# Kernel optimization log

Hardware: AMD Instinct MI355X
Metric: run time of the kernel (lower is better)

Reference implementation:

```python
import jax, jax.numpy as jnp
import numpy as np

LN_EPS = 1e-5


def setup_inputs() -> dict:
    key = jax.random.key(0)
    ks = jax.random.split(key, 6)
    B, S, D = 4, 4096, 2048
    Db = D // 4  # bottleneck_dim = n_embd // compression_ratio
    hidden = jax.random.normal(ks[0], (B, S, D), dtype=jnp.float32)
    # LayerNorm params (torch defaults: gamma=1, beta=0)
    ln_gamma = jnp.ones((D,), dtype=jnp.float32)
    ln_beta = jnp.zeros((D,), dtype=jnp.float32)
    # Linear weights, torch default init: U(-1/sqrt(fan_in), 1/sqrt(fan_in))
    bd_lim = 1.0 / np.sqrt(D)
    W_down = jax.random.uniform(ks[1], (D, Db), minval=-bd_lim, maxval=bd_lim, dtype=jnp.float32)
    b_down = jax.random.uniform(ks[2], (Db,), minval=-bd_lim, maxval=bd_lim, dtype=jnp.float32)
    bu_lim = 1.0 / np.sqrt(Db)
    W_up = jax.random.uniform(ks[3], (Db, D), minval=-bu_lim, maxval=bu_lim, dtype=jnp.float32)
    b_up = jax.random.uniform(ks[4], (D,), minval=-bu_lim, maxval=bu_lim, dtype=jnp.float32)
    alpha = jnp.array(0.01, dtype=jnp.float32)
    return {
        "hidden": hidden,
        "ln_gamma": ln_gamma,
        "ln_beta": ln_beta,
        "W_down": W_down,
        "b_down": b_down,
        "W_up": W_up,
        "b_up": b_up,
        "alpha": alpha,
        "layer_idx": 0,
    }


def reference(hidden, ln_gamma, ln_beta, W_down, b_down, W_up, b_up, alpha, layer_idx):
    # LayerNorm over last dim
    mu = jnp.mean(hidden, axis=-1, keepdims=True)
    var = jnp.mean(jnp.square(hidden - mu), axis=-1, keepdims=True)
    h_norm = (hidden - mu) * jax.lax.rsqrt(var + LN_EPS) * ln_gamma + ln_beta
    # down-proj -> SiLU -> up-proj   [b s d] @ [d k] -> [b s k] -> [b s d]
    z = jnp.einsum("bsd,dk->bsk", h_norm, W_down) + b_down
    z = jax.nn.silu(z)
    bottleneck_out = jnp.einsum("bsk,kd->bsd", z, W_up) + b_up
    # alpha-gated residual
    return hidden + alpha * (bottleneck_out - hidden)
```

## Files before the change

kernel.cpp:

```cpp
#include <hip/hip_runtime.h>

typedef __bf16 bf16x8 __attribute__((ext_vector_type(8)));
typedef __bf16 bf16x4 __attribute__((ext_vector_type(4)));
typedef float f32x4 __attribute__((ext_vector_type(4)));

#define S_BARRIER() asm volatile("s_barrier" ::: "memory")
#define WAITCNT_VM(n) asm volatile("s_waitcnt vmcnt(" #n ")" ::: "memory")
#define WAITCNT_LGKM0() asm volatile("s_waitcnt lgkmcnt(0)" ::: "memory")

__global__ __launch_bounds__(256) void prep_ln_kernel(
    const float* __restrict__ Wd, __bf16* __restrict__ Wtd,
    const float* __restrict__ Wu, __bf16* __restrict__ Wtu,
    const float* __restrict__ x, const float* __restrict__ g,
    const float* __restrict__ be, __bf16* __restrict__ y,
    int D, int Db, int ntiles) {
    if ((int)blockIdx.x < ntiles) {
        const float* W;
        __bf16* Wt;
        int K, N, tile;
        const int ntile_d = (Db / 32) * (D / 32);
        if ((int)blockIdx.x < ntile_d) {
            W = Wd; Wt = Wtd; K = D; N = Db; tile = blockIdx.x;
        } else {
            W = Wu; Wt = Wtu; K = Db; N = D; tile = blockIdx.x - ntile_d;
        }
        const int tn = tile % (N / 32), tk = tile / (N / 32);
        const int n0 = tn * 32, k0 = tk * 32;
        __shared__ float t[32][33];
        const int c = threadIdx.x & 31, r0 = threadIdx.x >> 5;
#pragma unroll
        for (int r = r0; r < 32; r += 8)
            t[r][c] = W[(size_t)(k0 + r) * N + n0 + c];
        __syncthreads();
#pragma unroll
        for (int r = r0; r < 32; r += 8)
            Wt[(size_t)(n0 + r) * K + k0 + c] = (__bf16)t[c][r];
        return;
    }
    const int t = threadIdx.x;
    const int wv = t >> 6, ln = t & 63;
    const size_t row = (size_t)(blockIdx.x - ntiles) * 4 + wv;
    const float4* xr = (const float4*)(x + row * (size_t)D);
    const int nv = D >> 3;
    float s = 0.f, ss = 0.f;
    for (int i = ln; i < nv; i += 64) {
        float4 v0 = xr[i * 2], v1 = xr[i * 2 + 1];
        s += v0.x + v0.y + v0.z + v0.w + v1.x + v1.y + v1.z + v1.w;
        ss += v0.x * v0.x + v0.y * v0.y + v0.z * v0.z + v0.w * v0.w +
              v1.x * v1.x + v1.y * v1.y + v1.z * v1.z + v1.w * v1.w;
    }
#pragma unroll
    for (int o = 32; o > 0; o >>= 1) {
        s += __shfl_xor(s, o);
        ss += __shfl_xor(ss, o);
    }
    const float mu = s / (float)D;
    const float rstd = rsqrtf(ss / (float)D - mu * mu + 1e-5f);
    const float4* gg = (const float4*)g;
    const float4* bb = (const float4*)be;
    bf16x8* yr = (bf16x8*)(y + row * (size_t)D);
    for (int i = ln; i < nv; i += 64) {
        float4 v0 = xr[i * 2], v1 = xr[i * 2 + 1];
        float4 g0 = gg[i * 2], g1 = gg[i * 2 + 1];
        float4 b0 = bb[i * 2], b1 = bb[i * 2 + 1];
        bf16x8 o;
        o[0] = (__bf16)((v0.x - mu) * rstd * g0.x + b0.x);
        o[1] = (__bf16)((v0.y - mu) * rstd * g0.y + b0.y);
        o[2] = (__bf16)((v0.z - mu) * rstd * g0.z + b0.z);
        o[3] = (__bf16)((v0.w - mu) * rstd * g0.w + b0.w);
        o[4] = (__bf16)((v1.x - mu) * rstd * g1.x + b1.x);
        o[5] = (__bf16)((v1.y - mu) * rstd * g1.y + b1.y);
        o[6] = (__bf16)((v1.z - mu) * rstd * g1.z + b1.z);
        o[7] = (__bf16)((v1.w - mu) * rstd * g1.w + b1.w);
        yr[i] = o;
    }
}

template <int EPI, int BM>
__global__ __launch_bounds__(256, 4) void gemm_bt(const __bf16* __restrict__ A,
                                                  const __bf16* __restrict__ Bt,
                                                  const float* __restrict__ bias,
                                                  const float* __restrict__ hid,
                                                  const float* __restrict__ alpha_p,
                                                  void* __restrict__ Cout,
                                                  int M, int N, int K) {
    constexpr int BN = 128, BK = 32;
    constexpr int WM = BM / 2;
    constexpr int MI = WM / 16;
    constexpr int GA = BM / 64;
    __shared__ __align__(16) __bf16 Ads[3][BM * BK];
    __shared__ __align__(16) __bf16 Bds[3][BN * BK];

    const int tid = threadIdx.x;
    const int wave = tid >> 6;
    const int lane = tid & 63;
    const int bn = blockIdx.x, bm = blockIdx.y;
    const int row0 = bm * BM, col0 = bn * BN;
    const int wr = wave >> 1, wc = wave & 1;

    f32x4 acc[MI][4] = {};

    const __bf16* Ag = A + (size_t)row0 * K;
    const __bf16* Bg = Bt + (size_t)col0 * K;
    const int lrow = lane >> 2;
    const int lk = ((lane & 3) ^ (lrow & 3)) * 8;

    const int c = lane & 15;
    const int q = lane >> 4;

    auto stage = [&](int k0, int b) {
#pragma unroll
        for (int p = 0; p < GA; ++p) {
            const int r = wave * (16 * GA) + p * 16;
            __builtin_amdgcn_global_load_lds(
                (__attribute__((address_space(1))) void*)(Ag + (size_t)(r + lrow) * K + k0 + lk),
                (__attribute__((address_space(3))) void*)(&Ads[b][r * BK]),
                16, 0, 0);
        }
#pragma unroll
        for (int p = 0; p < 2; ++p) {
            const int r = wave * 32 + p * 16;
            __builtin_amdgcn_global_load_lds(
                (__attribute__((address_space(1))) void*)(Bg + (size_t)(r + lrow) * K + k0 + lk),
                (__attribute__((address_space(3))) void*)(&Bds[b][r * BK]),
                16, 0, 0);
        }
    };

    const int nk = K / BK;
    stage(0, 0);
    if (nk > 1) stage(BK, 1);
    int cur = 0, pf = 2;
    for (int it = 0; it < nk; ++it) {
        if (it + 1 < nk) {
            if constexpr (GA == 2) WAITCNT_VM(4); else WAITCNT_VM(3);
        } else {
            WAITCNT_VM(0);
        }
        WAITCNT_LGKM0();
        S_BARRIER();
        if (it + 2 < nk) stage((it + 2) * BK, pf);

        bf16x8 afW[4], bfA[MI];
#pragma unroll
        for (int j = 0; j < 4; ++j) {
            const int rl = wc * 64 + j * 16 + c;
            afW[j] = *(const bf16x8*)(&Bds[cur][rl * BK + ((q ^ (c & 3)) * 8)]);
        }
#pragma unroll
        for (int i = 0; i < MI; ++i) {
            const int rl = wr * WM + i * 16 + c;
            bfA[i] = *(const bf16x8*)(&Ads[cur][rl * BK + ((q ^ (c & 3)) * 8)]);
        }
#pragma unroll
        for (int i = 0; i < MI; ++i)
#pragma unroll
            for (int j = 0; j < 4; ++j)
                acc[i][j] = __builtin_amdgcn_mfma_f32_16x16x32_bf16(afW[j], bfA[i],
                                                                    acc[i][j], 0, 0, 0);
        cur = (cur + 1 == 3) ? 0 : cur + 1;
        pf = (pf + 1 == 3) ? 0 : pf + 1;
    }

    float alpha = (EPI == 1) ? *alpha_p : 0.f;
#pragma unroll
    for (int i = 0; i < MI; ++i) {
        const int rowg = row0 + wr * WM + i * 16 + c;
#pragma unroll
        for (int j = 0; j < 4; ++j) {
            const int colb = col0 + wc * 64 + j * 16 + q * 4;
            const float4 bv = *(const float4*)(bias + colb);
            float v0 = acc[i][j][0] + bv.x;
            float v1 = acc[i][j][1] + bv.y;
            float v2 = acc[i][j][2] + bv.z;
            float v3 = acc[i][j][3] + bv.w;
            const size_t idx = (size_t)rowg * N + colb;
            if (EPI == 0) {
                bf16x4 o;
                o[0] = (__bf16)(v0 / (1.f + __expf(-v0)));
                o[1] = (__bf16)(v1 / (1.f + __expf(-v1)));
                o[2] = (__bf16)(v2 / (1.f + __expf(-v2)));
                o[3] = (__bf16)(v3 / (1.f + __expf(-v3)));
                *(bf16x4*)((__bf16*)Cout + idx) = o;
            } else {
                const float4 h = *(const float4*)(hid + idx);
                float4 o;
                o.x = h.x + alpha * (v0 - h.x);
                o.y = h.y + alpha * (v1 - h.y);
                o.z = h.z + alpha * (v2 - h.z);
                o.w = h.w + alpha * (v3 - h.w);
                *(float4*)((float*)Cout + idx) = o;
            }
        }
    }
}

extern "C" void kernel_launch(void* const* d_in, const int* in_sizes, int n_in,
                              void* d_out, int out_size, void* d_ws, size_t ws_size,
                              hipStream_t stream) {
    const float* hidden = (const float*)d_in[0];
    const float* ln_gamma = (const float*)d_in[1];
    const float* ln_beta = (const float*)d_in[2];
    const float* W_down = (const float*)d_in[3];
    const float* b_down = (const float*)d_in[4];
    const float* W_up = (const float*)d_in[5];
    const float* b_up = (const float*)d_in[6];
    const float* alpha = (const float*)d_in[7];
    float* out = (float*)d_out;

    const int D = in_sizes[2];
    const int Db = in_sizes[4];
    const int M = in_sizes[0] / D;

    char* w = (char*)d_ws;
    __bf16* hn = (__bf16*)w;  w += (size_t)M * D * sizeof(__bf16);
    __bf16* z = (__bf16*)w;   w += (size_t)M * Db * sizeof(__bf16);
    __bf16* Wtd = (__bf16*)w; w += (size_t)D * Db * sizeof(__bf16);
    __bf16* Wtu = (__bf16*)w; w += (size_t)Db * D * sizeof(__bf16);

    const int ntiles = 2 * (D / 32) * (Db / 32);
    prep_ln_kernel<<<ntiles + M / 4, 256, 0, stream>>>(W_down, Wtd, W_up, Wtu,
                                                       hidden, ln_gamma, ln_beta, hn,
                                                       D, Db, ntiles);

    gemm_bt<0, 64><<<dim3(Db / 128, M / 64), 256, 0, stream>>>(
        hn, Wtd, b_down, nullptr, nullptr, (void*)z, M, Db, D);

    gemm_bt<1, 128><<<dim3(D / 128, M / 128), 256, 0, stream>>>(
        z, Wtu, b_up, hidden, alpha, (void*)out, M, D, Db);
}
```

Before: 400.7 us.

## Replace LDS-staged GEMM with per-wave direct global-load MFMA GEMM; cache LN row in registers

The triple-buffered LDS GEMM, which staged tiles through LDS with global_load_lds and barriers, is replaced by a kernel where each wave independently owns a 64x32 or 64x64 output tile and loads MFMA operands straight from global memory into registers. This removes LDS traffic and block-wide barriers, but block-level operand sharing is gone, so cross-wave reuse now depends on L1/L2 and global load latency is exposed without explicit prefetch. The LayerNorm path also keeps the row in registers so the input is read once instead of twice. The register cache assumes D <= 4096.

After: 571.1 us. 42.5% more time.

```diff
diff --git a/kernel.cpp b/kernel.cpp
--- a/kernel.cpp
+++ b/kernel.cpp
@@ -3,10 +3,6 @@
 typedef __bf16 bf16x8 __attribute__((ext_vector_type(8)));
 typedef __bf16 bf16x4 __attribute__((ext_vector_type(4)));
 typedef float f32x4 __attribute__((ext_vector_type(4)));
-
-#define S_BARRIER() asm volatile("s_barrier" ::: "memory")
-#define WAITCNT_VM(n) asm volatile("s_waitcnt vmcnt(" #n ")" ::: "memory")
-#define WAITCNT_LGKM0() asm volatile("s_waitcnt lgkmcnt(0)" ::: "memory")
 
 __global__ __launch_bounds__(256) void prep_ln_kernel(
     const float* __restrict__ Wd, __bf16* __restrict__ Wtd,
@@ -42,12 +38,19 @@
     const size_t row = (size_t)(blockIdx.x - ntiles) * 4 + wv;
     const float4* xr = (const float4*)(x + row * (size_t)D);
     const int nv = D >> 3;
+    float4 xs[16];
     float s = 0.f, ss = 0.f;
-    for (int i = ln; i < nv; i += 64) {
-        float4 v0 = xr[i * 2], v1 = xr[i * 2 + 1];
-        s += v0.x + v0.y + v0.z + v0.w + v1.x + v1.y + v1.z + v1.w;
-        ss += v0.x * v0.x + v0.y * v0.y + v0.z * v0.z + v0.w * v0.w +
-              v1.x * v1.x + v1.y * v1.y + v1.z * v1.z + v1.w * v1.w;
+#pragma unroll
+    for (int ii = 0; ii < 8; ++ii) {
+        const int i = ii * 64 + ln;
+        if (i < nv) {
+            float4 v0 = xr[i * 2], v1 = xr[i * 2 + 1];
+            xs[2 * ii] = v0;
+            xs[2 * ii + 1] = v1;
+            s += v0.x + v0.y + v0.z + v0.w + v1.x + v1.y + v1.z + v1.w;
+            ss += v0.x * v0.x + v0.y * v0.y + v0.z * v0.z + v0.w * v0.w +
+                  v1.x * v1.x + v1.y * v1.y + v1.z * v1.z + v1.w * v1.w;
+        }
     }
 #pragma unroll
     for (int o = 32; o > 0; o >>= 1) {
@@ -59,116 +62,80 @@
     const float4* gg = (const float4*)g;
     const float4* bb = (const float4*)be;
     bf16x8* yr = (bf16x8*)(y + row * (size_t)D);
-    for (int i = ln; i < nv; i += 64) {
-        float4 v0 = xr[i * 2], v1 = xr[i * 2 + 1];
-        float4 g0 = gg[i * 2], g1 = gg[i * 2 + 1];
-        float4 b0 = bb[i * 2], b1 = bb[i * 2 + 1];
-        bf16x8 o;
-        o[0] = (__bf16)((v0.x - mu) * rstd * g0.x + b0.x);
-        o[1] = (__bf16)((v0.y - mu) * rstd * g0.y + b0.y);
-        o[2] = (__bf16)((v0.z - mu) * rstd * g0.z + b0.z);
-        o[3] = (__bf16)((v0.w - mu) * rstd * g0.w + b0.w);
-        o[4] = (__bf16)((v1.x - mu) * rstd * g1.x + b1.x);
-        o[5] = (__bf16)((v1.y - mu) * rstd * g1.y + b1.y);
-        o[6] = (__bf16)((v1.z - mu) * rstd * g1.z + b1.z);
-        o[7] = (__bf16)((v1.w - mu) * rstd * g1.w + b1.w);
-        yr[i] = o;
+#pragma unroll
+    for (int ii = 0; ii < 8; ++ii) {
+        const int i = ii * 64 + ln;
+        if (i < nv) {
+            float4 v0 = xs[2 * ii], v1 = xs[2 * ii + 1];
+            float4 g0 = gg[i * 2], g1 = gg[i * 2 + 1];
+            float4 b0 = bb[i * 2], b1 = bb[i * 2 + 1];
+            bf16x8 o;
+            o[0] = (__bf16)((v0.x - mu) * rstd * g0.x + b0.x);
+            o[1] = (__bf16)((v0.y - mu) * rstd * g0.y + b0.y);
+            o[2] = (__bf16)((v0.z - mu) * rstd * g0.z + b0.z);
+            o[3] = (__bf16)((v0.w - mu) * rstd * g0.w + b0.w);
+            o[4] = (__bf16)((v1.x - mu) * rstd * g1.x + b1.x);
+            o[5] = (__bf16)((v1.y - mu) * rstd * g1.y + b1.y);
+            o[6] = (__bf16)((v1.z - mu) * rstd * g1.z + b1.z);
+            o[7] = (__bf16)((v1.w - mu) * rstd * g1.w + b1.w);
+            yr[i] = o;
+        }
     }
 }
 
-template <int EPI, int BM>
-__global__ __launch_bounds__(256, 4) void gemm_bt(const __bf16* __restrict__ A,
-                                                  const __bf16* __restrict__ Bt,
-                                                  const float* __restrict__ bias,
-                                                  const float* __restrict__ hid,
-                                                  const float* __restrict__ alpha_p,
-                                                  void* __restrict__ Cout,
-                                                  int M, int N, int K) {
-    constexpr int BN = 128, BK = 32;
-    constexpr int WM = BM / 2;
-    constexpr int MI = WM / 16;
-    constexpr int GA = BM / 64;
-    __shared__ __align__(16) __bf16 Ads[3][BM * BK];
-    __shared__ __align__(16) __bf16 Bds[3][BN * BK];
-
-    const int tid = threadIdx.x;
-    const int wave = tid >> 6;
-    const int lane = tid & 63;
-    const int bn = blockIdx.x, bm = blockIdx.y;
-    const int row0 = bm * BM, col0 = bn * BN;
-    const int wr = wave >> 1, wc = wave & 1;
-
-    f32x4 acc[MI][4] = {};
-
-    const __bf16* Ag = A + (size_t)row0 * K;
-    const __bf16* Bg = Bt + (size_t)col0 * K;
-    const int lrow = lane >> 2;
-    const int lk = ((lane & 3) ^ (lrow & 3)) * 8;
-
+template <int EPI, int WM, int WN>
+__global__ __launch_bounds__(256, 3) void gemm_direct(
+    const __bf16* __restrict__ A, const __bf16* __restrict__ Bt,
+    const float* __restrict__ bias, const float* __restrict__ hid,
+    const float* __restrict__ alpha_p, void* __restrict__ Cout,
+    int M, int N, int K) {
+    constexpr int MI = WM / 16, NJ = WN / 16;
+    const int wave = threadIdx.x >> 6;
+    const int lane = threadIdx.x & 63;
+    const int wid = blockIdx.x * 4 + wave;
+    const int ntn = N / WN;
+    const int tm = wid / ntn, tn = wid % ntn;
+    const int row0 = tm * WM, col0 = tn * WN;
     const int c = lane & 15;
     const int q = lane >> 4;
 
-    auto stage = [&](int k0, int b) {
+    f32x4 acc[MI][NJ] = {};
+
+    const __bf16* pA[MI];
+    const __bf16* pB[NJ];
 #pragma unroll
-        for (int p = 0; p < GA; ++p) {
-            const int r = wave * (16 * GA) + p * 16;
-            __builtin_amdgcn_global_load_lds(
-                (__attribute__((address_space(1))) void*)(Ag + (size_t)(r + lrow) * K + k0 + lk),
-                (__attribute__((address_space(3))) void*)(&Ads[b][r * BK]),
-                16, 0, 0);
-        }
+    for (int i = 0; i < MI; ++i)
+        pA[i] = A + (size_t)(row0 + i * 16 + c) * K + q * 8;
 #pragma unroll
-        for (int p = 0; p < 2; ++p) {
-            const int r = wave * 32 + p * 16;
-            __builtin_amdgcn_global_load_lds(
-                (__attribute__((address_space(1))) void*)(Bg + (size_t)(r + lrow) * K + k0 + lk),
-                (__attribute__((address_space(3))) void*)(&Bds[b][r * BK]),
-                16, 0, 0);
-        }
-    };
+    for (int j = 0; j < NJ; ++j)
+        pB[j] = Bt + (size_t)(col0 + j * 16 + c) * K + q * 8;
 
-    const int nk = K / BK;
-    stage(0, 0);
-    if (nk > 1) stage(BK, 1);
-    int cur = 0, pf = 2;
+    const int nk = K / 32;
+#pragma unroll 4
     for (int it = 0; it < nk; ++it) {
-        if (it + 1 < nk) {
-            if constexpr (GA == 2) WAITCNT_VM(4); else WAITCNT_VM(3);
-        } else {
-            WAITCNT_VM(0);
-        }
-        WAITCNT_LGKM0();
-        S_BARRIER();
-        if (it + 2 < nk) stage((it + 2) * BK, pf);
-
-        bf16x8 afW[4], bfA[MI];
+        const int ko = it * 32;
+        bf16x8 af[NJ], bf_[MI];
 #pragma unroll
-        for (int j = 0; j < 4; ++j) {
-            const int rl = wc * 64 + j * 16 + c;
-            afW[j] = *(const bf16x8*)(&Bds[cur][rl * BK + ((q ^ (c & 3)) * 8)]);
-        }
+        for (int j = 0; j < NJ; ++j)
+            af[j] = *(const bf16x8*)(pB[j] + ko);
 #pragma unroll
-        for (int i = 0; i < MI; ++i) {
-            const int rl = wr * WM + i * 16 + c;
-            bfA[i] = *(const bf16x8*)(&Ads[cur][rl * BK + ((q ^ (c & 3)) * 8)]);
-        }
+        for (int i = 0; i < MI; ++i)
+            bf_[i] = *(const bf16x8*)(pA[i] + ko);
 #pragma unroll
         for (int i = 0; i < MI; ++i)
 #pragma unroll
-            for (int j = 0; j < 4; ++j)
-                acc[i][j] = __builtin_amdgcn_mfma_f32_16x16x32_bf16(afW[j], bfA[i],
+            for (int j = 0; j < NJ; ++j)
+                acc[i][j] = __builtin_amdgcn_mfma_f32_16x16x32_bf16(af[j], bf_[i],
                                                                     acc[i][j], 0, 0, 0);
-        cur = (cur + 1 == 3) ? 0 : cur + 1;
-        pf = (pf + 1 == 3) ? 0 : pf + 1;
     }
 
     float alpha = (EPI == 1) ? *alpha_p : 0.f;
 #pragma unroll
     for (int i = 0; i < MI; ++i) {
-        const int rowg = row0 + wr * WM + i * 16 + c;
+        const int rowg = row0 + i * 16 + c;
 #pragma unroll
-        for (int j = 0; j < 4; ++j) {
-            const int colb = col0 + wc * 64 + j * 16 + q * 4;
+        for (int j = 0; j < NJ; ++j) {
+            const int colb = col0 + j * 16 + q * 4;
             const float4 bv = *(const float4*)(bias + colb);
             float v0 = acc[i][j][0] + bv.x;
             float v1 = acc[i][j][1] + bv.y;
@@ -223,9 +190,9 @@
                                                        hidden, ln_gamma, ln_beta, hn,
                                                        D, Db, ntiles);
 
-    gemm_bt<0, 64><<<dim3(Db / 128, M / 64), 256, 0, stream>>>(
+    gemm_direct<0, 64, 32><<<(M / 64) * (Db / 32) / 4, 256, 0, stream>>>(
         hn, Wtd, b_down, nullptr, nullptr, (void*)z, M, Db, D);
 
-    gemm_bt<1, 128><<<dim3(D / 128, M / 128), 256, 0, stream>>>(
+    gemm_direct<1, 64, 64><<<(M / 64) * (D / 64) / 4, 256, 0, stream>>>(
         z, Wtu, b_up, hidden, alpha, (void*)out, M, D, Db);
 }
```

## Cache LayerNorm row in registers and switch GEMM to double-buffered pipeline

Applied to the files above, without the earlier changes.

The LayerNorm pass now keeps the loaded row in registers, so the input is not read from global memory a second time. The GEMM goes from a three-stage to a two-stage LDS ring: the next tile is issued before waiting, and a second barrier at the end of each iteration protects the buffer being reused. Templates now take BN and min-waves parameters, with the down-projection raised to 5 waves per SIMD, and the residual epilogue loads all hidden values before computing. The smaller LDS footprint may allow higher occupancy, but the shallower prefetch and extra barrier could expose more memory latency.

Result: faster. 392.6 us (-2.0%).

```diff
diff --git a/kernel.cpp b/kernel.cpp
--- a/kernel.cpp
+++ b/kernel.cpp
@@ -42,12 +42,19 @@
     const size_t row = (size_t)(blockIdx.x - ntiles) * 4 + wv;
     const float4* xr = (const float4*)(x + row * (size_t)D);
     const int nv = D >> 3;
+    float4 xs[16];
     float s = 0.f, ss = 0.f;
-    for (int i = ln; i < nv; i += 64) {
-        float4 v0 = xr[i * 2], v1 = xr[i * 2 + 1];
-        s += v0.x + v0.y + v0.z + v0.w + v1.x + v1.y + v1.z + v1.w;
-        ss += v0.x * v0.x + v0.y * v0.y + v0.z * v0.z + v0.w * v0.w +
-              v1.x * v1.x + v1.y * v1.y + v1.z * v1.z + v1.w * v1.w;
+#pragma unroll
+    for (int ii = 0; ii < 8; ++ii) {
+        const int i = ii * 64 + ln;
+        if (i < nv) {
+            float4 v0 = xr[i * 2], v1 = xr[i * 2 + 1];
+            xs[2 * ii] = v0;
+            xs[2 * ii + 1] = v1;
+            s += v0.x + v0.y + v0.z + v0.w + v1.x + v1.y + v1.z + v1.w;
+            ss += v0.x * v0.x + v0.y * v0.y + v0.z * v0.z + v0.w * v0.w +
+                  v1.x * v1.x + v1.y * v1.y + v1.z * v1.z + v1.w * v1.w;
+        }
     }
 #pragma unroll
     for (int o = 32; o > 0; o >>= 1) {
@@ -59,37 +66,40 @@
     const float4* gg = (const float4*)g;
     const float4* bb = (const float4*)be;
     bf16x8* yr = (bf16x8*)(y + row * (size_t)D);
-    for (int i = ln; i < nv; i += 64) {
-        float4 v0 = xr[i * 2], v1 = xr[i * 2 + 1];
-        float4 g0 = gg[i * 2], g1 = gg[i * 2 + 1];
-        float4 b0 = bb[i * 2], b1 = bb[i * 2 + 1];
-        bf16x8 o;
-        o[0] = (__bf16)((v0.x - mu) * rstd * g0.x + b0.x);
-        o[1] = (__bf16)((v0.y - mu) * rstd * g0.y + b0.y);
-        o[2] = (__bf16)((v0.z - mu) * rstd * g0.z + b0.z);
-        o[3] = (__bf16)((v0.w - mu) * rstd * g0.w + b0.w);
-        o[4] = (__bf16)((v1.x - mu) * rstd * g1.x + b1.x);
-        o[5] = (__bf16)((v1.y - mu) * rstd * g1.y + b1.y);
-        o[6] = (__bf16)((v1.z - mu) * rstd * g1.z + b1.z);
-        o[7] = (__bf16)((v1.w - mu) * rstd * g1.w + b1.w);
-        yr[i] = o;
+#pragma unroll
+    for (int ii = 0; ii < 8; ++ii) {
+        const int i = ii * 64 + ln;
+        if (i < nv) {
+            float4 v0 = xs[2 * ii], v1 = xs[2 * ii + 1];
+            float4 g0 = gg[i * 2], g1 = gg[i * 2 + 1];
+            float4 b0 = bb[i * 2], b1 = bb[i * 2 + 1];
+            bf16x8 o;
+            o[0] = (__bf16)((v0.x - mu) * rstd * g0.x + b0.x);
+            o[1] = (__bf16)((v0.y - mu) * rstd * g0.y + b0.y);
+            o[2] = (__bf16)((v0.z - mu) * rstd * g0.z + b0.z);
+            o[3] = (__bf16)((v0.w - mu) * rstd * g0.w + b0.w);
+            o[4] = (__bf16)((v1.x - mu) * rstd * g1.x + b1.x);
+            o[5] = (__bf16)((v1.y - mu) * rstd * g1.y + b1.y);
+            o[6] = (__bf16)((v1.z - mu) * rstd * g1.z + b1.z);
+            o[7] = (__bf16)((v1.w - mu) * rstd * g1.w + b1.w);
+            yr[i] = o;
+        }
     }
 }
 
-template <int EPI, int BM>
-__global__ __launch_bounds__(256, 4) void gemm_bt(const __bf16* __restrict__ A,
-                                                  const __bf16* __restrict__ Bt,
-                                                  const float* __restrict__ bias,
-                                                  const float* __restrict__ hid,
-                                                  const float* __restrict__ alpha_p,
-                                                  void* __restrict__ Cout,
-                                                  int M, int N, int K) {
-    constexpr int BN = 128, BK = 32;
-    constexpr int WM = BM / 2;
-    constexpr int MI = WM / 16;
-    constexpr int GA = BM / 64;
-    __shared__ __align__(16) __bf16 Ads[3][BM * BK];
-    __shared__ __align__(16) __bf16 Bds[3][BN * BK];
+template <int EPI, int BM, int BN, int MINW>
+__global__ __launch_bounds__(256, MINW) void gemm_bt(
+    const __bf16* __restrict__ A, const __bf16* __restrict__ Bt,
+    const float* __restrict__ bias, const float* __restrict__ hid,
+    const float* __restrict__ alpha_p, void* __restrict__ Cout,
+    int M, int N, int K) {
+    constexpr int BK = 32;
+    constexpr int WM = BM / 2, WN = BN / 2;
+    constexpr int MI = WM / 16, NJ = WN / 16;
+    constexpr int GA = BM / 64, GB = BN / 64;
+    constexpr int L = GA + GB;
+    __shared__ __align__(16) __bf16 Ads[2][BM * BK];
+    __shared__ __align__(16) __bf16 Bds[2][BN * BK];
 
     const int tid = threadIdx.x;
     const int wave = tid >> 6;
@@ -98,7 +108,7 @@
     const int row0 = bm * BM, col0 = bn * BN;
     const int wr = wave >> 1, wc = wave & 1;
 
-    f32x4 acc[MI][4] = {};
+    f32x4 acc[MI][NJ] = {};
 
     const __bf16* Ag = A + (size_t)row0 * K;
     const __bf16* Bg = Bt + (size_t)col0 * K;
@@ -118,8 +128,8 @@
                 16, 0, 0);
         }
 #pragma unroll
-        for (int p = 0; p < 2; ++p) {
-            const int r = wave * 32 + p * 16;
+        for (int p = 0; p < GB; ++p) {
+            const int r = wave * (16 * GB) + p * 16;
             __builtin_amdgcn_global_load_lds(
                 (__attribute__((address_space(1))) void*)(Bg + (size_t)(r + lrow) * K + k0 + lk),
                 (__attribute__((address_space(3))) void*)(&Bds[b][r * BK]),
@@ -129,22 +139,20 @@
 
     const int nk = K / BK;
     stage(0, 0);
-    if (nk > 1) stage(BK, 1);
-    int cur = 0, pf = 2;
     for (int it = 0; it < nk; ++it) {
+        const int cur = it & 1;
         if (it + 1 < nk) {
-            if constexpr (GA == 2) WAITCNT_VM(4); else WAITCNT_VM(3);
+            stage((it + 1) * BK, cur ^ 1);
+            if constexpr (L == 3) WAITCNT_VM(3); else WAITCNT_VM(4);
         } else {
             WAITCNT_VM(0);
         }
-        WAITCNT_LGKM0();
         S_BARRIER();
-        if (it + 2 < nk) stage((it + 2) * BK, pf);
-
-        bf16x8 afW[4], bfA[MI];
-#pragma unroll
-        for (int j = 0; j < 4; ++j) {
-            const int rl = wc * 64 + j * 16 + c;
+
+        bf16x8 afW[NJ], bfA[MI];
+#pragma unroll
+        for (int j = 0; j < NJ; ++j) {
+            const int rl = wc * WN + j * 16 + c;
             afW[j] = *(const bf16x8*)(&Bds[cur][rl * BK + ((q ^ (c & 3)) * 8)]);
         }
 #pragma unroll
@@ -155,41 +163,55 @@
 #pragma unroll
         for (int i = 0; i < MI; ++i)
 #pragma unroll
-            for (int j = 0; j < 4; ++j)
+            for (int j = 0; j < NJ; ++j)
                 acc[i][j] = __builtin_amdgcn_mfma_f32_16x16x32_bf16(afW[j], bfA[i],
                                                                     acc[i][j], 0, 0, 0);
-        cur = (cur + 1 == 3) ? 0 : cur + 1;
-        pf = (pf + 1 == 3) ? 0 : pf + 1;
+        WAITCNT_LGKM0();
+        S_BARRIER();
     }
 
     float alpha = (EPI == 1) ? *alpha_p : 0.f;
 #pragma unroll
     for (int i = 0; i < MI; ++i) {
         const int rowg = row0 + wr * WM + i * 16 + c;
-#pragma unroll
-        for (int j = 0; j < 4; ++j) {
-            const int colb = col0 + wc * 64 + j * 16 + q * 4;
-            const float4 bv = *(const float4*)(bias + colb);
-            float v0 = acc[i][j][0] + bv.x;
-            float v1 = acc[i][j][1] + bv.y;
-            float v2 = acc[i][j][2] + bv.z;
-            float v3 = acc[i][j][3] + bv.w;
-            const size_t idx = (size_t)rowg * N + colb;
-            if (EPI == 0) {
+        if (EPI == 0) {
+#pragma unroll
+            for (int j = 0; j < NJ; ++j) {
+                const int colb = col0 + wc * WN + j * 16 + q * 4;
+                const float4 bv = *(const float4*)(bias + colb);
+                float v0 = acc[i][j][0] + bv.x;
+                float v1 = acc[i][j][1] + bv.y;
+                float v2 = acc[i][j][2] + bv.z;
+                float v3 = acc[i][j][3] + bv.w;
+                const size_t idx = (size_t)rowg * N + colb;
                 bf16x4 o;
                 o[0] = (__bf16)(v0 / (1.f + __expf(-v0)));
                 o[1] = (__bf16)(v1 / (1.f + __expf(-v1)));
                 o[2] = (__bf16)(v2 / (1.f + __expf(-v2)));
                 o[3] = (__bf16)(v3 / (1.f + __expf(-v3)));
                 *(bf16x4*)((__bf16*)Cout + idx) = o;
-            } else {
-                const float4 h = *(const float4*)(hid + idx);
+            }
+        } else {
+            float4 hv[NJ];
+#pragma unroll
+            for (int j = 0; j < NJ; ++j) {
+                const int colb = col0 + wc * WN + j * 16 + q * 4;
+                hv[j] = *(const float4*)(hid + (size_t)rowg * N + colb);
+            }
+#pragma unroll
+            for (int j = 0; j < NJ; ++j) {
+                const int colb = col0 + wc * WN + j * 16 + q * 4;
+                const float4 bv = *(const float4*)(bias + colb);
+                float v0 = acc[i][j][0] + bv.x;
+                float v1 = acc[i][j][1] + bv.y;
+                float v2 = acc[i][j][2] + bv.z;
+                float v3 = acc[i][j][3] + bv.w;
                 float4 o;
-                o.x = h.x + alpha * (v0 - h.x);
-                o.y = h.y + alpha * (v1 - h.y);
-                o.z = h.z + alpha * (v2 - h.z);
-                o.w = h.w + alpha * (v3 - h.w);
-                *(float4*)((float*)Cout + idx) = o;
+                o.x = hv[j].x + alpha * (v0 - hv[j].x);
+                o.y = hv[j].y + alpha * (v1 - hv[j].y);
+                o.z = hv[j].z + alpha * (v2 - hv[j].z);
+                o.w = hv[j].w + alpha * (v3 - hv[j].w);
+                *(float4*)((float*)Cout + (size_t)rowg * N + colb) = o;
             }
         }
     }
@@ -223,9 +245,9 @@
                                                        hidden, ln_gamma, ln_beta, hn,
                                                        D, Db, ntiles);
 
-    gemm_bt<0, 64><<<dim3(Db / 128, M / 64), 256, 0, stream>>>(
+    gemm_bt<0, 64, 128, 5><<<dim3(Db / 128, M / 64), 256, 0, stream>>>(
         hn, Wtd, b_down, nullptr, nullptr, (void*)z, M, Db, D);
 
-    gemm_bt<1, 128><<<dim3(D / 128, M / 128), 256, 0, stream>>>(
+    gemm_bt<1, 128, 128, 4><<<dim3(D / 128, M / 128), 256, 0, stream>>>(
         z, Wtu, b_up, hidden, alpha, (void*)out, M, D, Db);
 }
```
